# Kernel tuning notes

Hardware: AMD Instinct MI355X
Metric: run time of the kernel (lower is better)

The kernel has to match this reference:

```python
import jax, jax.numpy as jnp
import numpy as np
import math

B, L, D, H, ITEMS = 256, 200, 64, 2, 10000
HEAD = D // H
LN_EPS = 1e-12


def setup_inputs() -> dict:
    key = jax.random.key(0)
    ks = jax.random.split(key, 12)
    x = jax.random.normal(ks[0], (B, L, D), dtype=jnp.float32)
    attention_mask = jnp.zeros((B, L, L), dtype=jnp.float32)
    # distinct item ids per sequence -> well-conditioned C_sub submatrices
    perm_keys = jax.random.split(ks[1], B)
    seq_item_ids = jax.vmap(lambda k: jax.random.permutation(k, ITEMS)[:L])(perm_keys).astype(jnp.int32)
    # PSD-ish diversity kernel: C = 0.1 * F F^T + I  (guarantees invertible submatrices)
    F = jax.random.normal(ks[2], (ITEMS, 16), dtype=jnp.float32)
    C_kernel = 0.1 * (F @ F.T) + jnp.eye(ITEMS, dtype=jnp.float32)
    s = 1.0 / math.sqrt(D)
    Wq = jax.random.normal(ks[3], (D, D), dtype=jnp.float32) * s
    bq = jnp.zeros((D,), dtype=jnp.float32)
    Wv = jax.random.normal(ks[4], (D, D), dtype=jnp.float32) * s
    bv = jnp.zeros((D,), dtype=jnp.float32)
    Wd = jax.random.normal(ks[5], (D, D), dtype=jnp.float32) * s
    bd = jnp.zeros((D,), dtype=jnp.float32)
    ln_gamma = jnp.ones((D,), dtype=jnp.float32)
    ln_beta = jnp.zeros((D,), dtype=jnp.float32)
    return {"input_tensor": x, "attention_mask": attention_mask,
            "seq_item_ids": seq_item_ids, "C_kernel": C_kernel,
            "Wq": Wq, "bq": bq, "Wv": Wv, "bv": bv, "Wd": Wd, "bd": bd,
            "ln_gamma": ln_gamma, "ln_beta": ln_beta}


def _layer_norm(x, gamma, beta):
    mu = jnp.mean(x, axis=-1, keepdims=True)
    var = jnp.mean(jnp.square(x - mu), axis=-1, keepdims=True)
    return gamma * (x - mu) / jnp.sqrt(var + LN_EPS) + beta


def reference(input_tensor, attention_mask, seq_item_ids, C_kernel,
              Wq, bq, Wv, bv, Wd, bd, ln_gamma, ln_beta):
    x = input_tensor
    S = x @ Wq.T + bq                                    # [B,L,D]
    S2 = S * S
    L_kernel = jnp.einsum('bld,bmd->blm', S2, S2)        # [B,L,L]
    # gather per-sequence diversity submatrix C_sub[b,i,j] = C[ids[b,i], ids[b,j]]
    C_sub = C_kernel[seq_item_ids[:, :, None], seq_item_ids[:, None, :]]
    eye = jnp.eye(L, dtype=x.dtype)
    C_inv = jnp.linalg.inv(C_sub + 1e-4 * eye)
    T = jnp.einsum('blk,bkm->blm', L_kernel, C_inv)      # [B,L,L]
    diag_T = jnp.diagonal(T, axis1=1, axis2=2)           # [B,L]
    # 2x2 determinants of all (i,j) pairs: T_ii*T_jj - T_ij*T_ji
    subdet = diag_T[:, :, None] * diag_T[:, None, :] - T * jnp.swapaxes(T, 1, 2)
    triu = jnp.triu(jnp.ones((L, L), dtype=x.dtype), k=1)
    denom = jnp.sum(subdet * triu, axis=(1, 2), keepdims=True)
    denom = jnp.maximum(denom, 1e-9)
    subprob = subdet / denom
    diag_matrix = diag_T[:, :, None] * eye               # diag_embed
    score = -(subprob + diag_matrix) / math.sqrt(HEAD)
    score = score + attention_mask
    attn = jax.nn.softmax(score, axis=-1)
    V = x @ Wv.T + bv
    ctx = jnp.einsum('blm,bmd->bld', attn, V)
    out = ctx @ Wd.T + bd
    return _layer_norm(out + x, ln_gamma, ln_beta)
```

## Files before the change

kernel.cpp:

```cpp
#include <hip/hip_runtime.h>
#include <hip/hip_bf16.h>
#include <math.h>

#define NB 256
#define LL 200
#define DD 64
#define ITEMS_N 10000
#define RANK 16
#define ALPHA 1.0001f
#define INV_ALPHA (1.0f/1.0001f)
#define INV_SQRT_HEAD 0.17677669529663687f

typedef __attribute__((ext_vector_type(8))) short short8v;
typedef __attribute__((ext_vector_type(4))) float f32x4;

static __device__ __forceinline__ unsigned short f2b(float f) {
    unsigned u = __float_as_uint(f);
    unsigned r = (u + 0x7fffu + ((u >> 16) & 1u)) >> 16;
    return (unsigned short)r;
}
static __device__ __forceinline__ unsigned f2b2(float a, float c) {
    unsigned r;
    asm("v_cvt_pk_bf16_f32 %0, %1, %2" : "=v"(r) : "v"(a), "v"(c));
    return r;
}
static __device__ __forceinline__ float b2f(unsigned short h) {
    return __uint_as_float(((unsigned)h) << 16);
}

#define OFF_A     0
#define OFF_TB    29952
#define OFF_CL32  (OFF_TB + 0)
#define OFF_U32   (OFF_TB + 4224)
#define OFF_UTL   (OFF_TB + 6400)
#define OFF_XB    (OFF_TB + 20000)
#define OFF_WQB   (OFF_TB + 49952)
#define OFF_WVB   (OFF_TB + 59168)
#define OFF_BQS   (OFF_TB + 68384)
#define OFF_BVS   (OFF_TB + 68640)
#define OFF_UL    126464
#define OFF_UB    139264
#define OFF_PB    145920
#define OFF_MAUG  (OFF_PB + 0)
#define OFF_MINVT (OFF_PB + 2112)
#define OFF_IDSL  (OFF_PB + 3392)
#define OFF_PIV   (OFF_PB + 4192)
#define OFF_INVSQ (OFF_PB + 4256)
#define OFF_IDP   (OFF_PB + 4320)
#define OFF_ZB    152576
#define OFF_UTH   OFF_ZB
#define OFF_DV    159744
#define OFF_RED   160576
#define OFF_SCAL  160704
#define OFF_ZPAD  160720
#define LDS_TOTAL 160784

__global__ __launch_bounds__(1024) void mega_kernel(
        const float* __restrict__ x,    const float* __restrict__ mask,
        const int*   __restrict__ ids,  const float* __restrict__ C,
        const float* __restrict__ Wq,   const float* __restrict__ bq,
        const float* __restrict__ Wv,   const float* __restrict__ bv,
        const float* __restrict__ Wd,   const float* __restrict__ bd,
        const float* __restrict__ gamma,const float* __restrict__ beta,
        unsigned short* __restrict__ Vg, float* __restrict__ out) {
    extern __shared__ char smem[];
    unsigned short* Abuf = (unsigned short*)(smem + OFF_A);
    unsigned short* Tb   = (unsigned short*)(smem + OFF_TB);
    float* Cl32  = (float*)(smem + OFF_CL32);
    float* U32l  = (float*)(smem + OFF_U32);
    unsigned short* xbu  = (unsigned short*)(smem + OFF_XB);
    unsigned short* Wqbu = (unsigned short*)(smem + OFF_WQB);
    unsigned short* Wvbu = (unsigned short*)(smem + OFF_WVB);
    float* bqs   = (float*)(smem + OFF_BQS);
    float* bvs   = (float*)(smem + OFF_BVS);
    float*          Ul   = (float*)(smem + OFF_UL);
    unsigned short* Wdb  = (unsigned short*)(smem + OFF_UL);
    unsigned short* Ub   = (unsigned short*)(smem + OFF_UB);
    unsigned short* Pb   = (unsigned short*)(smem + OFF_PB);
    unsigned short* Zb   = (unsigned short*)(smem + OFF_ZB);
    float* dv   = (float*)(smem + OFF_DV);
    float* red  = (float*)(smem + OFF_RED);
    float* scal = (float*)(smem + OFF_SCAL);
    const short8v* zpad = (const short8v*)(smem + OFF_ZPAD);
    int*   idsl  = (int*)(smem + OFF_IDSL);
    int*   pivots= (int*)(smem + OFF_PIV);
    float* invsqv= (float*)(smem + OFF_INVSQ);
    int*   idpv  = (int*)(smem + OFF_IDP);
    float* Maug  = (float*)(smem + OFF_MAUG);
    float* MinvT = (float*)(smem + OFF_MINVT);

    int t = threadIdx.x;
    int b = blockIdx.x;
    int wv_ = t >> 6, lane = t & 63, fr = lane & 15, g = lane >> 4;

    int ga_ = t >> 5, gc_ = t & 31;
    float cgv;
    {
        int ia = ids[b*LL + ga_];
        int ic = ids[b*LL + gc_];
        cgv = C[(size_t)ia*ITEMS_N + ic];
    }

    {
        float4 z4; z4.x = 0.f; z4.y = 0.f; z4.z = 0.f; z4.w = 0.f;
        float4* tz = (float4*)(smem + OFF_TB + 92800);
        for (int i = t; i < 232; i += 1024) tz[i] = z4;
        float4* zz = (float4*)Zb;
        for (int i = t; i < 448; i += 1024) zz[i] = z4;
        if (t < 4) ((float4*)(smem + OFF_ZPAD))[t] = z4;
        if (t < 64)  ((unsigned*)(smem + OFF_UB + 6400))[t] = 0;
        if (t < 192) {
            int s = t / 12, c2 = t - s*12;
            *(unsigned*)(smem + OFF_UTL + s*448 + 400 + c2*4) = 0;
        }
        for (int i = t; i < 288; i += 1024) ((unsigned*)(smem + OFF_XB + 28800))[i] = 0;
        const float4* x4p = (const float4*)(x + (size_t)b*12800);
        #pragma unroll
        for (int it2 = 0; it2 < 4; ++it2) {
            int i4 = t + it2*1024;
            if (i4 < 3200) {
                float4 v4 = x4p[i4];
                int r = i4 >> 4, k4 = (i4 & 15) << 2;
                *(uint2*)(xbu + r*72 + k4) =
                    make_uint2(f2b2(v4.x, v4.y), f2b2(v4.z, v4.w));
            }
        }
        {
            float4 q4 = ((const float4*)Wq)[t];
            float4 w4 = ((const float4*)Wv)[t];
            int d2 = t >> 4, k4 = (t & 15) << 2;
            *(uint2*)(Wqbu + d2*72 + k4) = make_uint2(f2b2(q4.x, q4.y), f2b2(q4.z, q4.w));
            *(uint2*)(Wvbu + d2*72 + k4) = make_uint2(f2b2(w4.x, w4.y), f2b2(w4.z, w4.w));
        }
        if (t < 64) { bqs[t] = bq[t]; bvs[t] = bv[t]; }
        if (t < LL) idsl[t] = ids[b*LL + t];
        Cl32[ga_*33 + gc_] = cgv;
    }
    __syncthreads();

    unsigned vpack[8];
    #pragma unroll
    for (int i = 0; i < 8; ++i) vpack[i] = 0;
    if (wv_ == 0) {
        int a = lane & 31;
        float diag = Cl32[a*33 + a] - 1.0f;
        float ur[16];
        int   mypiv = 0; float myinv = 0.f;
        bool  removed = false;
        #pragma unroll
        for (int s = 0; s < RANK; ++s) {
            float v = removed ? -3e38f : diag;
            int idx = a;
            #pragma unroll
            for (int off = 16; off > 0; off >>= 1) {
                float v2 = __shfl_xor(v, off);
                int   i2 = __shfl_xor(idx, off);
                if (v2 > v || (v2 == v && i2 < idx)) { v = v2; idx = i2; }
            }
            int p = idx; float dp = v;
            float iv = (dp < 1e-9f) ? 0.0f : (1.0f/sqrtf(dp));
            float c = Cl32[a*33 + p] - ((a == p) ? 1.0f : 0.0f);
            #pragma unroll
            for (int k = 0; k < s; ++k) {
                float upk = __shfl(ur[k], p);
                c -= ur[k] * upk;
            }
            float u = c * iv;
            ur[s] = u;
            diag -= u*u;
            if (a == p) removed = true;
            if (lane == s) { mypiv = p; myinv = iv; }
        }
        #pragma unroll
        for (int s = 0; s < RANK; ++s) U32l[a*17 + s] = ur[s];
        if (lane < 16) {
            pivots[lane] = mypiv;
            invsqv[lane] = myinv;
            idpv[lane]   = idsl[mypiv];
        }
    } else {
        #pragma unroll
        for (int it2 = 0; it2 < 4; ++it2) {
            int tile = (wv_ - 1) + 15*it2;
            if (tile < 52) {
                int R = tile >> 2, Dt = tile & 3;
                const char* ar = (const char*)smem + OFF_XB + (R*16 + fr)*144;
                const char* qr = (const char*)smem + OFF_WQB + (Dt*16 + fr)*144;
                const char* vr = (const char*)smem + OFF_WVB + (Dt*16 + fr)*144;
                short8v a0 = *(const short8v*)(ar + g*16);
                short8v a1 = *(const short8v*)(ar + 64 + g*16);
                f32x4 qa = {0.f,0.f,0.f,0.f};
                f32x4 va = {0.f,0.f,0.f,0.f};
                qa = __builtin_amdgcn_mfma_f32_16x16x32_bf16(a0, *(const short8v*)(qr + g*16), qa, 0,0,0);
                qa = __builtin_amdgcn_mfma_f32_16x16x32_bf16(a1, *(const short8v*)(qr + 64 + g*16), qa, 0,0,0);
                va = __builtin_amdgcn_mfma_f32_16x16x32_bf16(a0, *(const short8v*)(vr + g*16), va, 0,0,0);
                va = __builtin_amdgcn_mfma_f32_16x16x32_bf16(a1, *(const short8v*)(vr + 64 + g*16), va, 0,0,0);
                int col = Dt*16 + fr;
                float bqc = bqs[col], bvc = bvs[col];
                unsigned s01 = f2b2((qa[0]+bqc)*(qa[0]+bqc), (qa[1]+bqc)*(qa[1]+bqc));
                unsigned s23 = f2b2((qa[2]+bqc)*(qa[2]+bqc), (qa[3]+bqc)*(qa[3]+bqc));
                #pragma unroll
                for (int reg = 0; reg < 4; ++reg) {
                    int row = R*16 + g*4 + reg;
                    unsigned short sv = (unsigned short)
                        (((reg < 2 ? s01 : s23) >> ((reg & 1)*16)) & 0xffffu);
                    Abuf[row*72 + col] = (row < LL) ? sv : (unsigned short)0;
                }
                vpack[2*it2]     = f2b2(va[0] + bvc, va[1] + bvc);
                vpack[2*it2 + 1] = f2b2(va[2] + bvc, va[3] + bvc);
            }
        }
    }
    __syncthreads();

    #define LK_TILE(Ridx, Ccidx)                                               \
    {                                                                          \
        int R = (Ridx), Cc = (Ccidx);                                          \
        short8v a0 = *(const short8v*)((char*)Abuf + (R*16 + fr)*144 + g*16);  \
        short8v a1 = *(const short8v*)((char*)Abuf + (R*16 + fr)*144 + 64 + g*16); \
        short8v b0 = *(const short8v*)((char*)Abuf + (Cc*16 + fr)*144 + g*16); \
        short8v b1 = *(const short8v*)((char*)Abuf + (Cc*16 + fr)*144 + 64 + g*16); \
        f32x4 acc = {0.f, 0.f, 0.f, 0.f};                                      \
        acc = __builtin_amdgcn_mfma_f32_16x16x32_bf16(a0, b0, acc, 0, 0, 0);   \
        acc = __builtin_amdgcn_mfma_f32_16x16x32_bf16(a1, b1, acc, 0, 0, 0);   \
        int col = Cc*16 + fr, row0 = R*16 + g*4;                               \
        if (col < LL && row0 < LL) {                                           \
            *(uint2*)&Tb[col*232 + row0] =                                     \
                make_uint2(f2b2(acc[0], acc[1]), f2b2(acc[2], acc[3]));        \
        }                                                                      \
    }

    if (wv_ < 4) {
        if (t < LL) {
            float cg[16];
            if (t < 32) {
                #pragma unroll
                for (int s = 0; s < RANK; ++s) cg[s] = Cl32[t*33 + pivots[s]];
            } else {
                int myid = idsl[t];
                #pragma unroll
                for (int s = 0; s < RANK; ++s)
                    cg[s] = C[(size_t)idpv[s]*ITEMS_N + myid];
            }
            float ur[16];
            #pragma unroll
            for (int s = 0; s < RANK; ++s) {
                int p = pivots[s];
                float c = cg[s] - ((t == p) ? 1.0f : 0.0f);
                #pragma unroll
                for (int k = 0; k < s; ++k) c -= ur[k] * U32l[p*17 + k];
                ur[s] = c * invsqv[s];
            }
            unsigned short* Uth = (unsigned short*)(smem + OFF_UTH);
            unsigned short* Utl = (unsigned short*)(smem + OFF_UTL);
            unsigned hp[8];
            #pragma unroll
            for (int s2 = 0; s2 < 8; ++s2) hp[s2] = f2b2(ur[2*s2], ur[2*s2 + 1]);
            float4* ul4 = (float4*)&Ul[t*RANK];
            ul4[0] = make_float4(ur[0],  ur[1],  ur[2],  ur[3]);
            ul4[1] = make_float4(ur[4],  ur[5],  ur[6],  ur[7]);
            ul4[2] = make_float4(ur[8],  ur[9],  ur[10], ur[11]);
            ul4[3] = make_float4(ur[12], ur[13], ur[14], ur[15]);
            uint4* ub4 = (uint4*)&Ub[t*RANK];
            ub4[0] = make_uint4(hp[0], hp[1], hp[2], hp[3]);
            ub4[1] = make_uint4(hp[4], hp[5], hp[6], hp[7]);
            #pragma unroll
            for (int s = 0; s < RANK; ++s) {
                unsigned short hv = (unsigned short)((hp[s >> 1] >> ((s & 1)*16)) & 0xffffu);
                Uth[s*224 + t] = hv;
                Utl[s*224 + t] = f2b(ur[s] - b2f(hv));
            }
        }
    } else {
        for (int idx = (wv_ - 4); idx < 96; idx += 12)
            LK_TILE(idx % 13, 2 + idx/13);
    }
    __syncthreads();

    if (wv_ == 0) {
        const char* uh  = smem + OFF_UTH;
        const char* ul2 = smem + OFF_UTL;
        f32x4 macc = {0.f,0.f,0.f,0.f};
        #pragma unroll
        for (int kb = 0; kb < 7; ++kb) {
            short8v h  = *(const short8v*)(uh  + fr*448 + kb*64 + g*16);
            short8v l2 = *(const short8v*)(ul2 + fr*448 + kb*64 + g*16);
            macc = __builtin_amdgcn_mfma_f32_16x16x32_bf16(h,  h,  macc, 0,0,0);
            macc = __builtin_amdgcn_mfma_f32_16x16x32_bf16(h,  l2, macc, 0,0,0);
            macc = __builtin_amdgcn_mfma_f32_16x16x32_bf16(l2, h,  macc, 0,0,0);
        }
        #pragma unroll
        for (int reg = 0; reg < 4; ++reg) {
            int r = g*4 + reg;
            Maug[r*33 + fr] = macc[reg] + ((r == fr) ? ALPHA : 0.f);
        }
        float m_[16], inv_[16];
        int rl = lane & 15;
        #pragma unroll
        for (int c = 0; c < 16; ++c) {
            m_[c]   = Maug[rl*33 + c];
            inv_[c] = (rl == c) ? 1.0f : 0.0f;
        }
        #pragma unroll
        for (int s = 0; s < 16; ++s) {
            float pv = __shfl(m_[s], s);
            float pvinv = 1.0f / pv;
            float f = m_[s];
            #pragma unroll
            for (int c = 0; c < 16; ++c) {
                float prow = __shfl(m_[c], s) * pvinv;
                float pinv = __shfl(inv_[c], s) * pvinv;
                if (lane == s) { m_[c] = prow; inv_[c] = pinv; }
                else { m_[c] = fmaf(-f, prow, m_[c]); inv_[c] = fmaf(-f, pinv, inv_[c]); }
            }
        }
        if (lane < 16) {
            #pragma unroll
            for (int c = 0; c < 16; ++c) MinvT[c*20 + rl] = inv_[c];
        }
    } else {
        for (int i = t - 64; i < 2720; i += 960) {
            int r = 30 + (i >> 4), c2 = i & 15;
            *(unsigned*)(smem + OFF_TB + r*464 + 400 + c2*4) = 0;
        }
        for (int idx = 96 + (wv_ - 1); idx < 143; idx += 15)
            LK_TILE(idx % 13, 2 + idx/13);
    }
    __syncthreads();

    float4 wd4 = ((const float4*)Wd)[t];
    for (int idx = t; idx < LL*RANK; idx += 1024) {
        int i = idx >> 4, r = idx & 15;
        float acc = 0.f;
        #pragma unroll
        for (int k = 0; k < 16; ++k) acc = fmaf(Ul[i*RANK + k], MinvT[r*20 + k], acc);
        Zb[r*224 + i] = f2b(acc);
    }
    if (t < 480) {
        int r = t >> 4, c2 = t & 15;
        *(unsigned*)(smem + OFF_TB + r*464 + 400 + c2*4) = 0;
    }
    for (int u2 = wv_; u2 < 26; u2 += 16)
        LK_TILE(u2 % 13, u2 / 13);
    __syncthreads();

    float2 mkr0[7];
    {
        int sp = wv_;
        int l0 = sp*16 + g;
        const float* mbase = mask + (size_t)b*40000;
        #pragma unroll
        for (int e = 0; e < 7; ++e) {
            int m0 = 2*fr + 32*e;
            mkr0[e] = ((sp < 13) && (m0 < LL))
                ? *(const float2*)(mbase + (size_t)l0*200 + m0) : make_float2(0.f, 0.f);
        }
    }
    {
        unsigned short* Vt = Abuf;
        if (wv_ > 0) {
            #pragma unroll
            for (int it2 = 0; it2 < 4; ++it2) {
                int tile = (wv_ - 1) + 15*it2;
                if (tile < 52) {
                    int R = tile >> 2, Dt = tile & 3;
                    int row0 = R*16 + g*4;
                    if (row0 < LL) {
                        *(uint2*)&Vt[(Dt*16 + fr)*232 + row0] =
                            make_uint2(vpack[2*it2], vpack[2*it2 + 1]);
                    }
                }
            }
        }
        for (int i = t; i < 2048; i += 1024) {
            int d = i >> 5, mc = i & 31;
            Vt[d*232 + 200 + mc] = 0;
        }
        {
            int d2 = t >> 4, k4 = (t & 15) << 2;
            *(uint2*)(Wdb + d2*72 + k4) =
                make_uint2(f2b2(wd4.x, wd4.y), f2b2(wd4.z, wd4.w));
        }
    }
    for (int strip = wv_; strip < 13; strip += 16) {
        f32x4 acc = {0.f, 0.f, 0.f, 0.f};
        const char* arow = (const char*)Tb + (size_t)(strip*16 + fr)*464;
        const char* brow = (const char*)Zb + (size_t)fr*448;
        #pragma unroll
        for (int kt = 0; kt < 7; ++kt) {
            short8v a  = *(const short8v*)(arow + kt*64 + g*16);
            short8v bb = *(const short8v*)(brow + kt*64 + g*16);
            acc = __builtin_amdgcn_mfma_f32_16x16x32_bf16(a, bb, acc, 0, 0, 0);
        }
        #pragma unroll
        for (int reg = 0; reg < 4; ++reg) {
            int prow = strip*16 + g*4 + reg;
            Pb[prow*16 + fr] = f2b(acc[reg]);
        }
    }
    __syncthreads();

    float2 mkr1[7];
    {
        int sp = wv_;
        int l1 = sp*16 + 4 + g;
        const float* mbase = mask + (size_t)b*40000;
        #pragma unroll
        for (int e = 0; e < 7; ++e) {
            int m0 = 2*fr + 32*e;
            mkr1[e] = ((sp < 13) && (m0 < LL))
                ? *(const float2*)(mbase + (size_t)l1*200 + m0) : make_float2(0.f, 0.f);
        }
    }
    {
        float ps = 0.f, psd = 0.f;
        for (int u = wv_; u < 91; u += 16) {
            int R, Cc;
            if (u < 13) { R = u; Cc = u; }
            else {
                int q = u - 13, rr = 0;
                while (q >= 12 - rr) { q -= 12 - rr; ++rr; }
                R = rr; Cc = rr + 1 + q;
            }
            const short8v* pPR = (g < 2) ? (const short8v*)((const char*)Pb + (R*16 + fr)*32 + g*16) : zpad;
            const short8v* pUC = (g < 2) ? (const short8v*)((const char*)Ub + (Cc*16 + fr)*32 + g*16) : zpad;
            const short8v* pUR = (g < 2) ? (const short8v*)((const char*)Ub + (R*16 + fr)*32 + g*16) : zpad;
            const short8v* pPC = (g < 2) ? (const short8v*)((const char*)Pb + (Cc*16 + fr)*32 + g*16) : zpad;
            f32x4 acc1 = {0.f,0.f,0.f,0.f};
            f32x4 acc2 = {0.f,0.f,0.f,0.f};
            acc1 = __builtin_amdgcn_mfma_f32_16x16x32_bf16(*pPR, *pUC, acc1, 0,0,0);
            acc2 = __builtin_amdgcn_mfma_f32_16x16x32_bf16(*pUR, *pPC, acc2, 0,0,0);
            if (u < 13) {
                #pragma unroll
                for (int reg = 0; reg < 4; ++reg) {
                    int row = R*16 + g*4 + reg, col = Cc*16 + fr;
                    float lk = b2f(Tb[row*232 + col]);
                    float tvA = (lk - acc1[reg]) * INV_ALPHA;
                    float tvT = (lk - acc2[reg]) * INV_ALPHA;
                    if (row < LL && col < LL) {
                        float w = tvA * tvT;
                        Tb[row*232 + col] = f2b(w);
                        ps += w;
                        if (row == col) { dv[row] = tvA; psd += tvA; }
                    }
                }
            } else {
                int col = Cc*16 + fr;
                float w[4];
                #pragma unroll
                for (int reg = 0; reg < 4; ++reg) {
                    int row = R*16 + g*4 + reg;
                    float lk = b2f(Tb[row*232 + col]);
                    float tvA = (lk - acc1[reg]) * INV_ALPHA;
                    float tvT = (lk - acc2[reg]) * INV_ALPHA;
                    w[reg] = tvA * tvT;
                }
                uint2 pk = make_uint2(f2b2(w[0], w[1]), f2b2(w[2], w[3]));
                if (col < LL) {
                    #pragma unroll
                    for (int reg = 0; reg < 4; ++reg) {
                        int row = R*16 + g*4 + reg;
                        Tb[row*232 + col] = (unsigned short)
                            (((reg < 2 ? pk.x : pk.y) >> ((reg & 1)*16)) & 0xffffu);
                        ps += 2.0f * w[reg];
                    }
                    int row0 = R*16 + g*4;
                    *(uint2*)&Tb[col*232 + row0] = pk;
                }
            }
        }
        #pragma unroll
        for (int off = 32; off > 0; off >>= 1) {
            ps  += __shfl_xor(ps, off);
            psd += __shfl_xor(psd, off);
        }
        if (lane == 0) { red[wv_] = ps; red[16 + wv_] = psd; }
        __syncthreads();
        if (t == 0) {
            float s1 = 0.f, s2 = 0.f;
            for (int k = 0; k < 16; ++k) { s1 += red[k]; s2 += red[16 + k]; }
            float dn = fmaxf(0.5f*(s2*s2 - s1), 1e-9f);
            scal[0] = 1.0f / dn;
        }
        __syncthreads();
    }

    {
        const unsigned short* Vt = Abuf;
        float invden = scal[0];
        int sp = wv_;
        if (sp < 13) {
            float2 mkr2[7], mkr3[7];
            {
                const float* mbase = mask + (size_t)b*40000;
                int l2 = sp*16 + 8 + g, l3 = sp*16 + 12 + g;
                #pragma unroll
                for (int e = 0; e < 7; ++e) {
                    int m0 = 2*fr + 32*e;
                    bool mm = (m0 < LL);
                    mkr2[e] = (mm && l2 < LL) ? *(const float2*)(mbase + (size_t)l2*200 + m0) : make_float2(0.f, 0.f);
                    mkr3[e] = (mm && l3 < LL) ? *(const float2*)(mbase + (size_t)l3*200 + m0) : make_float2(0.f, 0.f);
                }
            }
            float bdv[4], gv[4], bev[4];
            #pragma unroll
            for (int d2 = 0; d2 < 4; ++d2) {
                bdv[d2] = bd[d2*16 + fr];
                gv[d2]  = gamma[d2*16 + fr];
                bev[d2] = beta[d2*16 + fr];
            }
            char* hb = smem + OFF_UB + wv_*1152;
            float2 dvv[7];
            #pragma unroll
            for (int e = 0; e < 7; ++e) {
                int m0 = 2*fr + 32*e;
                dvv[e] = (m0 < LL) ? *(const float2*)(dv + m0) : make_float2(0.f, 0.f);
            }
            auto dorow = [&](const float2 (&mk)[7], int l) {
                if (l < LL) {
                    float dl = dv[l];
                    float sc[14]; float mx = -3e38f;
                    #pragma unroll
                    for (int e = 0; e < 7; ++e) {
                        int m0 = 2*fr + 32*e;
                        if (m0 < LL) {
                            unsigned w2 = *(const unsigned*)((const char*)Tb + ((size_t)l*232 + m0)*2);
                            float w0 = b2f((unsigned short)(w2 & 0xffffu));
                            float w1 = b2f((unsigned short)(w2 >> 16));
                            float s0 = -(fmaf(dl, dvv[e].x, -w0)*invden
                                         + ((m0 == l) ? dl : 0.f))*INV_SQRT_HEAD + mk[e].x;
                            float s1 = -(fmaf(dl, dvv[e].y, -w1)*invden
                                         + ((m0 + 1 == l) ? dl : 0.f))*INV_SQRT_HEAD + mk[e].y;
                            sc[2*e] = s0; sc[2*e + 1] = s1;
                            mx = fmaxf(mx, fmaxf(s0, s1));
                        } else { sc[2*e] = -3e38f; sc[2*e + 1] = -3e38f; }
                    }
                    mx = fmaxf(mx, __shfl_xor(mx, 1));
                    mx = fmaxf(mx, __shfl_xor(mx, 2));
                    mx = fmaxf(mx, __shfl_xor(mx, 4));
                    mx = fmaxf(mx, __shfl_xor(mx, 8));
                    float sum = 0.f;
                    #pragma unroll
                    for (int e = 0; e < 7; ++e) {
                        int m0 = 2*fr + 32*e;
                        if (m0 < LL) {
                            float e0 = __expf(sc[2*e] - mx);
                            float e1 = __expf(sc[2*e + 1] - mx);
                            sc[2*e] = e0; sc[2*e + 1] = e1;
                            sum += e0 + e1;
                        }
                    }
                    sum += __shfl_xor(sum, 1);
                    sum += __shfl_xor(sum, 2);
                    sum += __shfl_xor(sum, 4);
                    sum += __shfl_xor(sum, 8);
                    float isum = 1.0f / sum;
                    #pragma unroll
                    for (int e = 0; e < 7; ++e) {
                        int m0 = 2*fr + 32*e;
                        if (m0 < LL) {
                            unsigned pw = f2b2(sc[2*e]*isum, sc[2*e + 1]*isum);
                            *(unsigned*)((char*)Tb + ((size_t)l*232 + m0)*2) = pw;
                        }
                    }
                }
            };
            dorow(mkr0, sp*16 + g);
            dorow(mkr1, sp*16 + 4 + g);
            dorow(mkr2, sp*16 + 8 + g);
            dorow(mkr3, sp*16 + 12 + g);
            float xp[16];
            #pragma unroll
            for (int d2 = 0; d2 < 4; ++d2)
                #pragma unroll
                for (int reg = 0; reg < 4; ++reg) {
                    int l = sp*16 + g*4 + reg;
                    xp[d2*4 + reg] = (l < LL)
                        ? x[((size_t)b*LL + l)*64 + d2*16 + fr] : 0.f;
                }
            f32x4 cacc[4];
            #pragma unroll
            for (int d2 = 0; d2 < 4; ++d2) { f32x4 z = {0.f,0.f,0.f,0.f}; cacc[d2] = z; }
            {
                const char* arow = (const char*)Tb + (size_t)(sp*16 + fr)*464;
                #pragma unroll
                for (int kt = 0; kt < 7; ++kt) {
                    short8v a = *(const short8v*)(arow + kt*64 + g*16);
                    #pragma unroll
                    for (int d2 = 0; d2 < 4; ++d2) {
                        short8v bb = *(const short8v*)((const char*)Vt + (d2*16 + fr)*464 + kt*64 + g*16);
                        cacc[d2] = __builtin_amdgcn_mfma_f32_16x16x32_bf16(a, bb, cacc[d2], 0, 0, 0);
                    }
                }
            }
            f32x4 oacc[4];
            #pragma unroll
            for (int d2 = 0; d2 < 4; ++d2) { f32x4 z = {0.f,0.f,0.f,0.f}; oacc[d2] = z; }
            #pragma unroll
            for (int h = 0; h < 2; ++h) {
                #pragma unroll
                for (int d2 = 0; d2 < 2; ++d2)
                    #pragma unroll
                    for (int reg = 0; reg < 4; ++reg)
                        *(unsigned short*)(hb + ((g*4 + reg)*36 + d2*16 + fr)*2) = f2b(cacc[h*2 + d2][reg]);
                short8v a = *(const short8v*)(hb + fr*72 + g*16);
                #pragma unroll
                for (int d2 = 0; d2 < 4; ++d2) {
                    short8v bb = *(const short8v*)((const char*)Wdb + (d2*16 + fr)*144 + h*64 + g*16);
                    oacc[d2] = __builtin_amdgcn_mfma_f32_16x16x32_bf16(a, bb, oacc[d2], 0, 0, 0);
                }
            }
            #pragma unroll
            for (int reg = 0; reg < 4; ++reg) {
                int l = sp*16 + g*4 + reg;
                if (l < LL) {
                    float z0 = oacc[0][reg] + bdv[0] + xp[reg];
                    float z1 = oacc[1][reg] + bdv[1] + xp[4 + reg];
                    float z2 = oacc[2][reg] + bdv[2] + xp[8 + reg];
                    float z3 = oacc[3][reg] + bdv[3] + xp[12 + reg];
                    float s = z0 + z1 + z2 + z3;
                    s += __shfl_xor(s, 1); s += __shfl_xor(s, 2);
                    s += __shfl_xor(s, 4); s += __shfl_xor(s, 8);
                    float mu = s * (1.0f/64.0f);
                    float c0 = z0 - mu, c1 = z1 - mu, c2 = z2 - mu, c3 = z3 - mu;
                    float vs = c0*c0 + c1*c1 + c2*c2 + c3*c3;
                    vs += __shfl_xor(vs, 1); vs += __shfl_xor(vs, 2);
                    vs += __shfl_xor(vs, 4); vs += __shfl_xor(vs, 8);
                    float rstd = rsqrtf(vs * (1.0f/64.0f) + 1e-12f);
                    float* op = out + ((size_t)b*LL + l)*64 + fr;
                    op[0]  = fmaf(gv[0]*rstd, c0, bev[0]);
                    op[16] = fmaf(gv[1]*rstd, c1, bev[1]);
                    op[32] = fmaf(gv[2]*rstd, c2, bev[2]);
                    op[48] = fmaf(gv[3]*rstd, c3, bev[3]);
                }
            }
        }
    }
    #undef LK_TILE
}

extern "C" void kernel_launch(void* const* d_in, const int* in_sizes, int n_in,
                              void* d_out, int out_size, void* d_ws, size_t ws_size,
                              hipStream_t stream) {
    const float* x     = (const float*)d_in[0];
    const float* mask  = (const float*)d_in[1];
    const int*   ids   = (const int*)  d_in[2];
    const float* C     = (const float*)d_in[3];
    const float* Wq    = (const float*)d_in[4];
    const float* bq    = (const float*)d_in[5];
    const float* Wv    = (const float*)d_in[6];
    const float* bv    = (const float*)d_in[7];
    const float* Wd    = (const float*)d_in[8];
    const float* bd    = (const float*)d_in[9];
    const float* gamma = (const float*)d_in[10];
    const float* beta  = (const float*)d_in[11];
    float* out = (float*)d_out;

    unsigned short* Vb = (unsigned short*)d_ws;

    mega_kernel<<<NB, 1024, LDS_TOTAL, stream>>>(x, mask, ids, C, Wq, bq, Wv, bv,
                                                 Wd, bd, gamma, beta, Vb, out);
}
```

Measured before the change: 63.33 us.

## Spread softmax rows across all 16 waves and vectorize symmetric Tb reads

The softmax rows were handled only by waves 0-12, each taking 16 rows. They are now split across all 16 waves in interleaved groups of 4 rows, with a block barrier added before the context/output matmuls that only waves 0-12 run. This should remove idle waves during the exp/reduction phase. The subdet loop also reads the four Tb values from the transposed location with one 8-byte load instead of four scalar loads, relying on the symmetry of the L_kernel tile. The cost is an extra __syncthreads.

```diff
diff --git a/kernel.cpp b/kernel.cpp
--- a/kernel.cpp
+++ b/kernel.cpp
@@ -346,13 +346,12 @@
 
     float2 mkr0[7];
     {
-        int sp = wv_;
-        int l0 = sp*16 + g;
+        int l0 = wv_*4 + g;
         const float* mbase = mask + (size_t)b*40000;
         #pragma unroll
         for (int e = 0; e < 7; ++e) {
             int m0 = 2*fr + 32*e;
-            mkr0[e] = ((sp < 13) && (m0 < LL))
+            mkr0[e] = (m0 < LL)
                 ? *(const float2*)(mbase + (size_t)l0*200 + m0) : make_float2(0.f, 0.f);
         }
     }
@@ -402,13 +401,12 @@
 
     float2 mkr1[7];
     {
-        int sp = wv_;
-        int l1 = sp*16 + 4 + g;
+        int l1 = 64 + wv_*4 + g;
         const float* mbase = mask + (size_t)b*40000;
         #pragma unroll
         for (int e = 0; e < 7; ++e) {
             int m0 = 2*fr + 32*e;
-            mkr1[e] = ((sp < 13) && (m0 < LL))
+            mkr1[e] = (m0 < LL)
                 ? *(const float2*)(mbase + (size_t)l1*200 + m0) : make_float2(0.f, 0.f);
         }
     }
@@ -430,11 +428,14 @@
             f32x4 acc2 = {0.f,0.f,0.f,0.f};
             acc1 = __builtin_amdgcn_mfma_f32_16x16x32_bf16(*pPR, *pUC, acc1, 0,0,0);
             acc2 = __builtin_amdgcn_mfma_f32_16x16x32_bf16(*pUR, *pPC, acc2, 0,0,0);
+            int col = Cc*16 + fr, row0 = R*16 + g*4;
+            uint2 lk2 = *(const uint2*)&Tb[col*232 + row0];
             if (u < 13) {
                 #pragma unroll
                 for (int reg = 0; reg < 4; ++reg) {
-                    int row = R*16 + g*4 + reg, col = Cc*16 + fr;
-                    float lk = b2f(Tb[row*232 + col]);
+                    int row = row0 + reg;
+                    float lk = b2f((unsigned short)
+                        (((reg < 2 ? lk2.x : lk2.y) >> ((reg & 1)*16)) & 0xffffu));
                     float tvA = (lk - acc1[reg]) * INV_ALPHA;
                     float tvT = (lk - acc2[reg]) * INV_ALPHA;
                     if (row < LL && col < LL) {
@@ -445,12 +446,11 @@
                     }
                 }
             } else {
-                int col = Cc*16 + fr;
                 float w[4];
                 #pragma unroll
                 for (int reg = 0; reg < 4; ++reg) {
-                    int row = R*16 + g*4 + reg;
-                    float lk = b2f(Tb[row*232 + col]);
+                    float lk = b2f((unsigned short)
+                        (((reg < 2 ? lk2.x : lk2.y) >> ((reg & 1)*16)) & 0xffffu));
                     float tvA = (lk - acc1[reg]) * INV_ALPHA;
                     float tvT = (lk - acc2[reg]) * INV_ALPHA;
                     w[reg] = tvA * tvT;
@@ -459,12 +459,11 @@
                 if (col < LL) {
                     #pragma unroll
                     for (int reg = 0; reg < 4; ++reg) {
-                        int row = R*16 + g*4 + reg;
+                        int row = row0 + reg;
                         Tb[row*232 + col] = (unsigned short)
                             (((reg < 2 ? pk.x : pk.y) >> ((reg & 1)*16)) & 0xffffu);
                         ps += 2.0f * w[reg];
                     }
-                    int row0 = R*16 + g*4;
                     *(uint2*)&Tb[col*232 + row0] = pk;
                 }
             }
@@ -488,20 +487,91 @@
     {
         const unsigned short* Vt = Abuf;
         float invden = scal[0];
-        int sp = wv_;
-        if (sp < 13) {
-            float2 mkr2[7], mkr3[7];
-            {
-                const float* mbase = mask + (size_t)b*40000;
-                int l2 = sp*16 + 8 + g, l3 = sp*16 + 12 + g;
+        float2 mkr2[7], mkr3[7];
+        {
+            const float* mbase = mask + (size_t)b*40000;
+            int l2 = 128 + wv_*4 + g;
+            int l3 = 192 + wv_*4 + g;
+            bool p3 = (wv_ < 2);
+            #pragma unroll
+            for (int e = 0; e < 7; ++e) {
+                int m0 = 2*fr + 32*e;
+                bool mm = (m0 < LL);
+                mkr2[e] = mm         ? *(const float2*)(mbase + (size_t)l2*200 + m0) : make_float2(0.f, 0.f);
+                mkr3[e] = (mm && p3) ? *(const float2*)(mbase + (size_t)l3*200 + m0) : make_float2(0.f, 0.f);
+            }
+        }
+        float2 dvv[7];
+        #pragma unroll
+        for (int e = 0; e < 7; ++e) {
+            int m0 = 2*fr + 32*e;
+            dvv[e] = (m0 < LL) ? *(const float2*)(dv + m0) : make_float2(0.f, 0.f);
+        }
+        auto dorow = [&](const float2 (&mk)[7], int l) {
+            if (l < LL) {
+                float dl = dv[l];
+                float sc[14]; float mx = -3e38f;
                 #pragma unroll
                 for (int e = 0; e < 7; ++e) {
                     int m0 = 2*fr + 32*e;
-                    bool mm = (m0 < LL);
-                    mkr2[e] = (mm && l2 < LL) ? *(const float2*)(mbase + (size_t)l2*200 + m0) : make_float2(0.f, 0.f);
-                    mkr3[e] = (mm && l3 < LL) ? *(const float2*)(mbase + (size_t)l3*200 + m0) : make_float2(0.f, 0.f);
-                }
-            }
+                    if (m0 < LL) {
+                        unsigned w2 = *(const unsigned*)((const char*)Tb + ((size_t)l*232 + m0)*2);
+                        float w0 = b2f((unsigned short)(w2 & 0xffffu));
+                        float w1 = b2f((unsigned short)(w2 >> 16));
+                        float s0 = -(fmaf(dl, dvv[e].x, -w0)*invden
+                                     + ((m0 == l) ? dl : 0.f))*INV_SQRT_HEAD + mk[e].x;
+                        float s1 = -(fmaf(dl, dvv[e].y, -w1)*invden
+                                     + ((m0 + 1 == l) ? dl : 0.f))*INV_SQRT_HEAD + mk[e].y;
+                        sc[2*e] = s0; sc[2*e + 1] = s1;
+                        mx = fmaxf(mx, fmaxf(s0, s1));
+                    } else { sc[2*e] = -3e38f; sc[2*e + 1] = -3e38f; }
+                }
+                mx = fmaxf(mx, __shfl_xor(mx, 1));
+                mx = fmaxf(mx, __shfl_xor(mx, 2));
+                mx = fmaxf(mx, __shfl_xor(mx, 4));
+                mx = fmaxf(mx, __shfl_xor(mx, 8));
+                float sum = 0.f;
+                #pragma unroll
+                for (int e = 0; e < 7; ++e) {
+                    int m0 = 2*fr + 32*e;
+                    if (m0 < LL) {
+                        float e0 = __expf(sc[2*e] - mx);
+                        float e1 = __expf(sc[2*e + 1] - mx);
+                        sc[2*e] = e0; sc[2*e + 1] = e1;
+                        sum += e0 + e1;
+                    }
+                }
+                sum += __shfl_xor(sum, 1);
+                sum += __shfl_xor(sum, 2);
+                sum += __shfl_xor(sum, 4);
+                sum += __shfl_xor(sum, 8);
+                float isum = 1.0f / sum;
+                #pragma unroll
+                for (int e = 0; e < 7; ++e) {
+                    int m0 = 2*fr + 32*e;
+                    if (m0 < LL) {
+                        unsigned pw = f2b2(sc[2*e]*isum, sc[2*e + 1]*isum);
+                        *(unsigned*)((char*)Tb + ((size_t)l*232 + m0)*2) = pw;
+                    }
+                }
+            }
+        };
+        dorow(mkr0, wv_*4 + g);
+        dorow(mkr1, 64 + wv_*4 + g);
+        dorow(mkr2, 128 + wv_*4 + g);
+        if (wv_ < 2) dorow(mkr3, 192 + wv_*4 + g);
+        int sp = wv_;
+        float xp[16];
+        #pragma unroll
+        for (int d2 = 0; d2 < 4; ++d2)
+            #pragma unroll
+            for (int reg = 0; reg < 4; ++reg) {
+                int l = sp*16 + g*4 + reg;
+                xp[d2*4 + reg] = (sp < 13 && l < LL)
+                    ? x[((size_t)b*LL + l)*64 + d2*16 + fr] : 0.f;
+            }
+        __syncthreads();
+        if (sp < 13) {
             float bdv[4], gv[4], bev[4];
             #pragma unroll
             for (int d2 = 0; d2 < 4; ++d2) {
@@ -510,74 +580,6 @@
                 bev[d2] = beta[d2*16 + fr];
             }
             char* hb = smem + OFF_UB + wv_*1152;
-            float2 dvv[7];
-            #pragma unroll
-            for (int e = 0; e < 7; ++e) {
-                int m0 = 2*fr + 32*e;
-                dvv[e] = (m0 < LL) ? *(const float2*)(dv + m0) : make_float2(0.f, 0.f);
-            }
-            auto dorow = [&](const float2 (&mk)[7], int l) {
-                if (l < LL) {
-                    float dl = dv[l];
-                    float sc[14]; float mx = -3e38f;
-                    #pragma unroll
-                    for (int e = 0; e < 7; ++e) {
-                        int m0 = 2*fr + 32*e;
-                        if (m0 < LL) {
-                            unsigned w2 = *(const unsigned*)((const char*)Tb + ((size_t)l*232 + m0)*2);
-                            float w0 = b2f((unsigned short)(w2 & 0xffffu));
-                            float w1 = b2f((unsigned short)(w2 >> 16));
-                            float s0 = -(fmaf(dl, dvv[e].x, -w0)*invden
-                                         + ((m0 == l) ? dl : 0.f))*INV_SQRT_HEAD + mk[e].x;
-                            float s1 = -(fmaf(dl, dvv[e].y, -w1)*invden
-                                         + ((m0 + 1 == l) ? dl : 0.f))*INV_SQRT_HEAD + mk[e].y;
-                            sc[2*e] = s0; sc[2*e + 1] = s1;
-                            mx = fmaxf(mx, fmaxf(s0, s1));
-                        } else { sc[2*e] = -3e38f; sc[2*e + 1] = -3e38f; }
-                    }
-                    mx = fmaxf(mx, __shfl_xor(mx, 1));
-                    mx = fmaxf(mx, __shfl_xor(mx, 2));
-                    mx = fmaxf(mx, __shfl_xor(mx, 4));
-                    mx = fmaxf(mx, __shfl_xor(mx, 8));
-                    float sum = 0.f;
-                    #pragma unroll
-                    for (int e = 0; e < 7; ++e) {
-                        int m0 = 2*fr + 32*e;
-                        if (m0 < LL) {
-                            float e0 = __expf(sc[2*e] - mx);
-                            float e1 = __expf(sc[2*e + 1] - mx);
-                            sc[2*e] = e0; sc[2*e + 1] = e1;
-                            sum += e0 + e1;
-                        }
-                    }
-                    sum += __shfl_xor(sum, 1);
-                    sum += __shfl_xor(sum, 2);
-                    sum += __shfl_xor(sum, 4);
-                    sum += __shfl_xor(sum, 8);
-                    float isum = 1.0f / sum;
-                    #pragma unroll
-                    for (int e = 0; e < 7; ++e) {
-                        int m0 = 2*fr + 32*e;
-                        if (m0 < LL) {
-                            unsigned pw = f2b2(sc[2*e]*isum, sc[2*e + 1]*isum);
-                            *(unsigned*)((char*)Tb + ((size_t)l*232 + m0)*2) = pw;
-                        }
-                    }
-                }
-            };
-            dorow(mkr0, sp*16 + g);
-            dorow(mkr1, sp*16 + 4 + g);
-            dorow(mkr2, sp*16 + 8 + g);
-            dorow(mkr3, sp*16 + 12 + g);
-            float xp[16];
-            #pragma unroll
-            for (int d2 = 0; d2 < 4; ++d2)
-                #pragma unroll
-                for (int reg = 0; reg < 4; ++reg) {
-                    int l = sp*16 + g*4 + reg;
-                    xp[d2*4 + reg] = (l < LL)
-                        ? x[((size_t)b*LL + l)*64 + d2*16 + fr] : 0.f;
-                }
             f32x4 cacc[4];
             #pragma unroll
             for (int d2 = 0; d2 < 4; ++d2) { f32x4 z = {0.f,0.f,0.f,0.f}; cacc[d2] = z; }
```

Measured after the change: 62.03 us. 2.0% less time.
